# Kernel optimization log

Hardware: AMD Instinct MI355X
Metric: run time of the kernel (lower is better)

Reference implementation:

```python
import jax, jax.numpy as jnp
import numpy as np

RGB2GRAY = jnp.array([0.299, 0.587, 0.114], dtype=jnp.float32)


def _trilinear_slice(grid, z, y, x):
    """grid: (F, L, GH, GW); z,y,x: (H, W) float positions in index space
    (align_corners=True convention). Returns (H, W, F)."""
    F_, L, GH, GW = grid.shape
    z = jnp.clip(z, 0.0, L - 1)
    y = jnp.clip(y, 0.0, GH - 1)
    x = jnp.clip(x, 0.0, GW - 1)
    z0 = jnp.floor(z).astype(jnp.int32); z1 = jnp.minimum(z0 + 1, L - 1)
    y0 = jnp.floor(y).astype(jnp.int32); y1 = jnp.minimum(y0 + 1, GH - 1)
    x0 = jnp.floor(x).astype(jnp.int32); x1 = jnp.minimum(x0 + 1, GW - 1)
    wz = (z - z0)[..., None]  # (H, W, 1)
    wy = (y - y0)[..., None]
    wx = (x - x0)[..., None]

    def g(zi, yi, xi):  # gather corner -> (H, W, F)
        return jnp.moveaxis(grid[:, zi, yi, xi], 0, -1)

    c00 = g(z0, y0, x0) * (1 - wx) + g(z0, y0, x1) * wx
    c01 = g(z0, y1, x0) * (1 - wx) + g(z0, y1, x1) * wx
    c10 = g(z1, y0, x0) * (1 - wx) + g(z1, y0, x1) * wx
    c11 = g(z1, y1, x0) * (1 - wx) + g(z1, y1, x1) * wx
    c0 = c00 * (1 - wy) + c01 * wy
    c1 = c10 * (1 - wy) + c11 * wy
    return c0 * (1 - wz) + c1 * wz


def setup_inputs() -> dict:
    key = jax.random.key(0)
    k = jax.random.split(key, 5)
    H, W = 1080, 1920
    N, F_, L, GH, GW = 50, 16, 8, 16, 16
    hidden = 64
    rgb = jax.random.uniform(k[0], (H, W, 3), dtype=jnp.float32)
    grids = jax.random.normal(k[1], (N, F_, L, GH, GW), dtype=jnp.float32) * 0.1
    W1 = jax.random.normal(k[2], (hidden, F_), dtype=jnp.float32) * (1.0 / np.sqrt(F_))
    W2 = jax.random.normal(k[3], (hidden, hidden), dtype=jnp.float32) * (1.0 / np.sqrt(hidden))
    W3 = jax.random.normal(k[4], (12, hidden), dtype=jnp.float32) * (1.0 / np.sqrt(hidden))
    return {"rgb": rgb, "grids": grids, "W1": W1, "W2": W2, "W3": W3, "cam_idx": 3}


def reference(rgb, grids, W1, W2, W3, cam_idx):
    H, W, _ = rgb.shape
    _, F_, L, GH, GW = grids.shape
    grid = grids[cam_idx]  # (F, L, GH, GW)
    # guidance: gray in [0,1]; grid_sample coords in [-1,1] with align_corners=True
    # map directly to index space: pos = coord01 * (size - 1)
    gray = jnp.clip(jnp.tensordot(rgb, RGB2GRAY, axes=([-1], [0])), 0.0, 1.0)  # (H, W)
    gy = jnp.linspace(0.0, 1.0, H, dtype=jnp.float32)[:, None]  # (H, 1)
    gx = jnp.linspace(0.0, 1.0, W, dtype=jnp.float32)[None, :]  # (1, W)
    z = gray * (L - 1)
    y = jnp.broadcast_to(gy * (GH - 1), (H, W))
    x = jnp.broadcast_to(gx * (GW - 1), (H, W))
    feat = _trilinear_slice(grid, z, y, x)  # (H, W, F)
    # tiny per-pixel MLP (bias-free, torch Linear applies x @ W.T)
    h = jnp.tanh(feat @ W1.T)
    h = jnp.tanh(h @ W2.T)
    out = h @ W3.T  # (H, W, 12)
    return out.reshape(1, H, W, 3, 4)
```

## Files before the change

### kernel.cpp

```cpp
#include <hip/hip_runtime.h>

#define H_IMG 1080
#define W_IMG 1920
#define NPIX (H_IMG * W_IMG)

typedef __attribute__((ext_vector_type(8))) short bfrag8;
typedef __attribute__((ext_vector_type(4))) float facc4;

#define PK2_OFF 131072
#define PK3_OFF 147456
#define PK1_OFF 151552

__device__ __forceinline__ void split_bf16(float x, unsigned short& hi, unsigned short& lo) {
    unsigned xu = __float_as_uint(x);
    hi = (unsigned short)(xu >> 16);
    float hif = __uint_as_float(xu & 0xffff0000u);
    float lof = x - hif;
    lo = (unsigned short)(__float_as_uint(lof) >> 16);
}

__global__ void prep_kernel(const float* __restrict__ grids,
                            const int* __restrict__ cam_idx,
                            const float* __restrict__ W1,
                            const float* __restrict__ W2,
                            const float* __restrict__ W3,
                            float* __restrict__ grid_t,
                            unsigned short* __restrict__ pk1,
                            unsigned short* __restrict__ pk2,
                            unsigned short* __restrict__ pk3) {
    int idx = blockIdx.x * 256 + threadIdx.x;
    {
        int f = idx & 15, x = (idx >> 4) & 15, y = (idx >> 8) & 15, z = (idx >> 12) & 7;
        int cam = cam_idx[0];
        grid_t[idx] = grids[(((cam * 16 + f) * 8 + z) * 16 + y) * 16 + x];
    }
    if (idx < 8192) {
        int i = idx & 7, lane = (idx >> 3) & 63, h = (idx >> 9) & 1,
            s = (idx >> 10) & 1, mt = (idx >> 11) & 3;
        int j = mt * 16 + (lane & 15);
        int k = s * 32 + (lane >> 4) * 8 + i;
        unsigned short hi, lo;
        split_bf16(W2[j * 64 + k], hi, lo);
        pk2[idx] = h ? lo : hi;
    } else if (idx < 10240) {
        int e = idx - 8192;
        int i = e & 7, lane = (e >> 3) & 63, h = (e >> 9) & 1, s = (e >> 10) & 1;
        int c = lane & 15;
        int k = s * 32 + (lane >> 4) * 8 + i;
        float x = (c < 12) ? W3[c * 64 + k] : 0.0f;
        unsigned short hi, lo;
        split_bf16(x, hi, lo);
        pk3[e] = h ? lo : hi;
    } else if (idx < 14336) {
        int e = idx - 10240;
        int i = e & 7, lane = (e >> 3) & 63, h = (e >> 9) & 1, mt = (e >> 10) & 3;
        int j = mt * 16 + (lane & 15);
        int k = (lane >> 4) * 8 + i;
        float x = (k < 16) ? W1[j * 16 + k] : 0.0f;
        unsigned short hi, lo;
        split_bf16(x, hi, lo);
        pk1[e] = h ? lo : hi;
    }
}

__device__ __forceinline__ float fast_tanh(float x) {
    float e = exp2f(x * 2.8853900817779268f);
    return 1.0f - 2.0f * __builtin_amdgcn_rcpf(e + 1.0f);
}

__device__ __forceinline__ unsigned rtn_pair(float e, float o) {
    unsigned ue = __float_as_uint(e) + 0x8000u;
    unsigned uo = __float_as_uint(o) + 0x8000u;
    return __builtin_amdgcn_perm(uo, ue, 0x07060302u);
}

#define DS_FENCE() asm volatile("s_waitcnt lgkmcnt(0)" ::: "memory")
#define CBAR() asm volatile("" ::: "memory")
#define MFMA16(A, B, C) __builtin_amdgcn_mfma_f32_16x16x32_bf16((A), (B), (C), 0, 0, 0)

__global__ __launch_bounds__(256, 3)
void nbat_main(const float* __restrict__ rgb,
               const float* __restrict__ grid_t,
               const unsigned short* __restrict__ pk1,
               const unsigned short* __restrict__ pk2,
               const unsigned short* __restrict__ pk3,
               float* __restrict__ out) {
    __shared__ __align__(16) unsigned hbuf[4][3072];

    const int tid = threadIdx.x;
    const int w = tid >> 6, l = tid & 63;
    const int g = l >> 4, cc = l & 15;
    unsigned* hb = hbuf[w];
    uint4* hb4 = (uint4*)hb;
    const int H4 = 256;

    const int pixbase = blockIdx.x * 256 + w * 64;
    const int pix = pixbase + l;
    const int row = pix / W_IMG;
    const int col = pix - row * W_IMG;

    float r = rgb[3 * pix + 0];
    float gch = rgb[3 * pix + 1];
    float b = rgb[3 * pix + 2];
    float gray = fminf(fmaxf(0.299f * r + 0.587f * gch + 0.114f * b, 0.0f), 1.0f);

    float z = fminf(fmaxf(gray * 7.0f, 0.0f), 7.0f);
    float y = (float)row * (15.0f / 1079.0f);
    float x = (float)col * (15.0f / 1919.0f);

    float zf = floorf(z), yf = floorf(y), xf = floorf(x);
    int z0 = (int)zf, y0 = (int)yf, x0 = (int)xf;
    int z1 = min(z0 + 1, 7), y1 = min(y0 + 1, 15), x1 = min(x0 + 1, 15);
    float wz = z - zf, wy = y - yf, wx = x - xf;

    float feat[16];
#pragma unroll
    for (int i = 0; i < 16; ++i) feat[i] = 0.0f;

    const float4* gt4 = (const float4*)grid_t;
#pragma unroll
    for (int cz = 0; cz < 2; ++cz) {
        int zz = cz ? z1 : z0;
        float wwz = cz ? wz : (1.0f - wz);
#pragma unroll
        for (int cy = 0; cy < 2; ++cy) {
            int yy = cy ? y1 : y0;
            float wwzy = wwz * (cy ? wy : (1.0f - wy));
#pragma unroll
            for (int cx = 0; cx < 2; ++cx) {
                int xx = cx ? x1 : x0;
                float wc = wwzy * (cx ? wx : (1.0f - wx));
                int base = ((zz * 16 + yy) * 16 + xx) * 4;
#pragma unroll
                for (int q = 0; q < 4; ++q) {
                    float4 v = gt4[base + q];
                    feat[4 * q + 0] = fmaf(wc, v.x, feat[4 * q + 0]);
                    feat[4 * q + 1] = fmaf(wc, v.y, feat[4 * q + 1]);
                    feat[4 * q + 2] = fmaf(wc, v.z, feat[4 * q + 2]);
                    feat[4 * q + 3] = fmaf(wc, v.w, feat[4 * q + 3]);
                }
            }
        }
    }

    const int sl = (l >> 1) & 3;
    {
        uint4 q0, q1;
        q0.x = rtn_pair(feat[0], feat[1]);
        q0.y = rtn_pair(feat[2], feat[3]);
        q0.z = rtn_pair(feat[4], feat[5]);
        q0.w = rtn_pair(feat[6], feat[7]);
        q1.x = rtn_pair(feat[8], feat[9]);
        q1.y = rtn_pair(feat[10], feat[11]);
        q1.z = rtn_pair(feat[12], feat[13]);
        q1.w = rtn_pair(feat[14], feat[15]);
        uint4 zz4 = make_uint4(0u, 0u, 0u, 0u);
        hb4[l * 4 + (0 ^ sl)] = q0;
        hb4[l * 4 + (1 ^ sl)] = q1;
        hb4[l * 4 + (2 ^ sl)] = zz4;
        hb4[l * 4 + (3 ^ sl)] = zz4;
    }
    DS_FENCE();

    auto trans = [&](const facc4& v, int mt, int prow, int ubase)
        __attribute__((always_inline)) {
        float t0 = fast_tanh(v[0]);
        float t1 = fast_tanh(v[1]);
        float t2 = fast_tanh(v[2]);
        float t3 = fast_tanh(v[3]);
        unsigned A = rtn_pair(t0, t1);
        unsigned B = rtn_pair(t2, t3);
        int c = 2 * mt + (g >> 1);
        int u = ubase + prow * 32 + (((c ^ (prow & 7)) << 2) + ((g & 1) << 1));
        *(uint2*)(hb + u) = make_uint2(A, B);
    };

    const bfrag8* pk1v = (const bfrag8*)pk1;
    facc4 acc1[4][4];
#pragma unroll
    for (int mt = 0; mt < 4; ++mt)
#pragma unroll
        for (int nt = 0; nt < 4; ++nt) acc1[mt][nt] = (facc4){0.f, 0.f, 0.f, 0.f};
    {
        bfrag8 w1h[4], w1l[4];
#pragma unroll
        for (int mt = 0; mt < 4; ++mt) {
            w1h[mt] = pk1v[(mt * 2 + 0) * 64 + l];
            w1l[mt] = pk1v[(mt * 2 + 1) * 64 + l];
        }
#pragma unroll
        for (int nt = 0; nt < 4; ++nt) {
            int p = cc + 16 * nt;
            uint4 bq = hb4[p * 4 + (g ^ ((p >> 1) & 3))];
            bfrag8 bf = __builtin_bit_cast(bfrag8, bq);
#pragma unroll
            for (int mt = 0; mt < 4; ++mt) {
                acc1[mt][nt] = MFMA16(w1l[mt], bf, acc1[mt][nt]);
                acc1[mt][nt] = MFMA16(w1h[mt], bf, acc1[mt][nt]);
            }
        }
    }

#pragma unroll
    for (int mt = 0; mt < 4; ++mt)
#pragma unroll
        for (int nt = 0; nt < 4; ++nt) trans(acc1[mt][nt], mt, cc + 16 * nt, 1024);
    DS_FENCE();

    const bfrag8* pk2v = (const bfrag8*)pk2;
    const bfrag8* pk3v = (const bfrag8*)pk3;
#pragma unroll
    for (int h = 0; h < 2; ++h) {
        facc4 acc2[4][2];
#pragma unroll
        for (int mt = 0; mt < 4; ++mt)
#pragma unroll
            for (int ntl = 0; ntl < 2; ++ntl) acc2[mt][ntl] = (facc4){0.f, 0.f, 0.f, 0.f};
#pragma unroll
        for (int s = 0; s < 2; ++s) {
            bfrag8 w2h[4], w2l[4];
#pragma unroll
            for (int mt = 0; mt < 4; ++mt) {
                w2h[mt] = pk2v[((mt * 2 + s) * 2 + 0) * 64 + l];
                w2l[mt] = pk2v[((mt * 2 + s) * 2 + 1) * 64 + l];
            }
#pragma unroll
            for (int ntl = 0; ntl < 2; ++ntl) {
                int p = cc + 16 * (2 * h + ntl);
                uint4 q = hb4[H4 + p * 8 + ((4 * s + g) ^ (p & 7))];
                bfrag8 bh = __builtin_bit_cast(bfrag8, q);
#pragma unroll
                for (int mt = 0; mt < 4; ++mt) {
                    acc2[mt][ntl] = MFMA16(w2l[mt], bh, acc2[mt][ntl]);
                    acc2[mt][ntl] = MFMA16(w2h[mt], bh, acc2[mt][ntl]);
                }
            }
        }

#pragma unroll
        for (int mt = 0; mt < 4; ++mt)
#pragma unroll
            for (int ntl = 0; ntl < 2; ++ntl) trans(acc2[mt][ntl], mt, cc + 16 * ntl, 0);
        DS_FENCE();

        facc4 o3[2];
#pragma unroll
        for (int ntl = 0; ntl < 2; ++ntl) o3[ntl] = (facc4){0.f, 0.f, 0.f, 0.f};
#pragma unroll
        for (int s = 0; s < 2; ++s) {
            bfrag8 w3h = pk3v[(s * 2 + 0) * 64 + l];
            bfrag8 w3l = pk3v[(s * 2 + 1) * 64 + l];
#pragma unroll
            for (int ntl = 0; ntl < 2; ++ntl) {
                int pl = cc + 16 * ntl;
                uint4 q = hb4[pl * 8 + ((4 * s + g) ^ (pl & 7))];
                bfrag8 bh = __builtin_bit_cast(bfrag8, q);
                o3[ntl] = MFMA16(w3l, bh, o3[ntl]);
                o3[ntl] = MFMA16(w3h, bh, o3[ntl]);
            }
        }

        if (g < 3) {
#pragma unroll
            for (int ntl = 0; ntl < 2; ++ntl) {
                int p = pixbase + 32 * h + 16 * ntl + cc;
                *(float4*)(out + p * 12 + 4 * g) =
                    make_float4(o3[ntl][0], o3[ntl][1], o3[ntl][2], o3[ntl][3]);
            }
        }
        CBAR();
    }
}

extern "C" void kernel_launch(void* const* d_in, const int* in_sizes, int n_in,
                              void* d_out, int out_size, void* d_ws, size_t ws_size,
                              hipStream_t stream) {
    const float* rgb   = (const float*)d_in[0];
    const float* grids = (const float*)d_in[1];
    const float* W1    = (const float*)d_in[2];
    const float* W2    = (const float*)d_in[3];
    const float* W3    = (const float*)d_in[4];
    const int*   cam   = (const int*)d_in[5];

    float* grid_t = (float*)d_ws;
    unsigned short* pk2 = (unsigned short*)((char*)d_ws + PK2_OFF);
    unsigned short* pk3 = (unsigned short*)((char*)d_ws + PK3_OFF);
    unsigned short* pk1 = (unsigned short*)((char*)d_ws + PK1_OFF);

    hipLaunchKernelGGL(prep_kernel, dim3(128), dim3(256), 0, stream,
                       grids, cam, W1, W2, W3, grid_t, pk1, pk2, pk3);
    hipLaunchKernelGGL(nbat_main, dim3(NPIX / 256), dim3(256), 0, stream,
                       rgb, grid_t, pk1, pk2, pk3, (float*)d_out);
}
```

Before: 181.7 us.

## Halve pixels per wave, shrink LDS, raise occupancy, add MFMA priority hints

Each wave now handles 32 pixels instead of 64. Only half the lanes compute the trilinear features, and the two-half layer-2/3 loop is removed. The LDS buffer is halved, launch bounds go from 3 to 4 waves per SIMD, and the grid doubles. s_setprio wraps the MFMA bursts so waves in their matrix phase get issue priority. The goal is more waves in flight to hide latency, at the cost of idle lanes during the gather, twice the weight-fragment reloads per pixel, and more blocks.

```diff
diff --git a/kernel.cpp b/kernel.cpp
--- a/kernel.cpp
+++ b/kernel.cpp
@@ -75,76 +75,78 @@
 }
 
 #define DS_FENCE() asm volatile("s_waitcnt lgkmcnt(0)" ::: "memory")
-#define CBAR() asm volatile("" ::: "memory")
 #define MFMA16(A, B, C) __builtin_amdgcn_mfma_f32_16x16x32_bf16((A), (B), (C), 0, 0, 0)
-
-__global__ __launch_bounds__(256, 3)
+#define PRIO_HI() __builtin_amdgcn_s_setprio(1)
+#define PRIO_LO() __builtin_amdgcn_s_setprio(0)
+
+__global__ __launch_bounds__(256, 4)
 void nbat_main(const float* __restrict__ rgb,
                const float* __restrict__ grid_t,
                const unsigned short* __restrict__ pk1,
                const unsigned short* __restrict__ pk2,
                const unsigned short* __restrict__ pk3,
                float* __restrict__ out) {
-    __shared__ __align__(16) unsigned hbuf[4][3072];
+    __shared__ __align__(16) unsigned hbuf[4][1536];
 
     const int tid = threadIdx.x;
     const int w = tid >> 6, l = tid & 63;
     const int g = l >> 4, cc = l & 15;
     unsigned* hb = hbuf[w];
     uint4* hb4 = (uint4*)hb;
-    const int H4 = 256;
-
-    const int pixbase = blockIdx.x * 256 + w * 64;
-    const int pix = pixbase + l;
-    const int row = pix / W_IMG;
-    const int col = pix - row * W_IMG;
-
-    float r = rgb[3 * pix + 0];
-    float gch = rgb[3 * pix + 1];
-    float b = rgb[3 * pix + 2];
-    float gray = fminf(fmaxf(0.299f * r + 0.587f * gch + 0.114f * b, 0.0f), 1.0f);
-
-    float z = fminf(fmaxf(gray * 7.0f, 0.0f), 7.0f);
-    float y = (float)row * (15.0f / 1079.0f);
-    float x = (float)col * (15.0f / 1919.0f);
-
-    float zf = floorf(z), yf = floorf(y), xf = floorf(x);
-    int z0 = (int)zf, y0 = (int)yf, x0 = (int)xf;
-    int z1 = min(z0 + 1, 7), y1 = min(y0 + 1, 15), x1 = min(x0 + 1, 15);
-    float wz = z - zf, wy = y - yf, wx = x - xf;
-
-    float feat[16];
-#pragma unroll
-    for (int i = 0; i < 16; ++i) feat[i] = 0.0f;
-
-    const float4* gt4 = (const float4*)grid_t;
-#pragma unroll
-    for (int cz = 0; cz < 2; ++cz) {
-        int zz = cz ? z1 : z0;
-        float wwz = cz ? wz : (1.0f - wz);
-#pragma unroll
-        for (int cy = 0; cy < 2; ++cy) {
-            int yy = cy ? y1 : y0;
-            float wwzy = wwz * (cy ? wy : (1.0f - wy));
-#pragma unroll
-            for (int cx = 0; cx < 2; ++cx) {
-                int xx = cx ? x1 : x0;
-                float wc = wwzy * (cx ? wx : (1.0f - wx));
-                int base = ((zz * 16 + yy) * 16 + xx) * 4;
-#pragma unroll
-                for (int q = 0; q < 4; ++q) {
-                    float4 v = gt4[base + q];
-                    feat[4 * q + 0] = fmaf(wc, v.x, feat[4 * q + 0]);
-                    feat[4 * q + 1] = fmaf(wc, v.y, feat[4 * q + 1]);
-                    feat[4 * q + 2] = fmaf(wc, v.z, feat[4 * q + 2]);
-                    feat[4 * q + 3] = fmaf(wc, v.w, feat[4 * q + 3]);
+    const int HT4 = 128;
+
+    const int pixbase = blockIdx.x * 128 + w * 32;
+
+    if (l < 32) {
+        const int pix = pixbase + l;
+        const int row = pix / W_IMG;
+        const int col = pix - row * W_IMG;
+
+        float r = rgb[3 * pix + 0];
+        float gch = rgb[3 * pix + 1];
+        float b = rgb[3 * pix + 2];
+        float gray = fminf(fmaxf(0.299f * r + 0.587f * gch + 0.114f * b, 0.0f), 1.0f);
+
+        float z = fminf(fmaxf(gray * 7.0f, 0.0f), 7.0f);
+        float y = (float)row * (15.0f / 1079.0f);
+        float x = (float)col * (15.0f / 1919.0f);
+
+        float zf = floorf(z), yf = floorf(y), xf = floorf(x);
+        int z0 = (int)zf, y0 = (int)yf, x0 = (int)xf;
+        int z1 = min(z0 + 1, 7), y1 = min(y0 + 1, 15), x1 = min(x0 + 1, 15);
+        float wz = z - zf, wy = y - yf, wx = x - xf;
+
+        float feat[16];
+#pragma unroll
+        for (int i = 0; i < 16; ++i) feat[i] = 0.0f;
+
+        const float4* gt4 = (const float4*)grid_t;
+#pragma unroll
+        for (int cz = 0; cz < 2; ++cz) {
+            int zz = cz ? z1 : z0;
+            float wwz = cz ? wz : (1.0f - wz);
+#pragma unroll
+            for (int cy = 0; cy < 2; ++cy) {
+                int yy = cy ? y1 : y0;
+                float wwzy = wwz * (cy ? wy : (1.0f - wy));
+#pragma unroll
+                for (int cx = 0; cx < 2; ++cx) {
+                    int xx = cx ? x1 : x0;
+                    float wc = wwzy * (cx ? wx : (1.0f - wx));
+                    int base = ((zz * 16 + yy) * 16 + xx) * 4;
+#pragma unroll
+                    for (int q = 0; q < 4; ++q) {
+                        float4 v = gt4[base + q];
+                        feat[4 * q + 0] = fmaf(wc, v.x, feat[4 * q + 0]);
+                        feat[4 * q + 1] = fmaf(wc, v.y, feat[4 * q + 1]);
+                        feat[4 * q + 2] = fmaf(wc, v.z, feat[4 * q + 2]);
+                        feat[4 * q + 3] = fmaf(wc, v.w, feat[4 * q + 3]);
+                    }
                 }
             }
         }
-    }
-
-    const int sl = (l >> 1) & 3;
-    {
+
+        const int sl = (l >> 1) & 3;
         uint4 q0, q1;
         q0.x = rtn_pair(feat[0], feat[1]);
         q0.y = rtn_pair(feat[2], feat[3]);
@@ -162,25 +164,35 @@
     }
     DS_FENCE();
 
-    auto trans = [&](const facc4& v, int mt, int prow, int ubase)
-        __attribute__((always_inline)) {
+    bfrag8 bf[2];
+#pragma unroll
+    for (int nt = 0; nt < 2; ++nt) {
+        int p = cc + 16 * nt;
+        bf[nt] = __builtin_bit_cast(bfrag8, hb4[p * 4 + (g ^ ((p >> 1) & 3))]);
+    }
+
+    auto trans = [&](const facc4& v, int mt, int ntl) __attribute__((always_inline)) {
         float t0 = fast_tanh(v[0]);
         float t1 = fast_tanh(v[1]);
         float t2 = fast_tanh(v[2]);
         float t3 = fast_tanh(v[3]);
         unsigned A = rtn_pair(t0, t1);
         unsigned B = rtn_pair(t2, t3);
+        int p = cc + 16 * ntl;
         int c = 2 * mt + (g >> 1);
-        int u = ubase + prow * 32 + (((c ^ (prow & 7)) << 2) + ((g & 1) << 1));
+        int u = 512 + p * 32 + (((c ^ (p & 7)) << 2) + ((g & 1) << 1));
         *(uint2*)(hb + u) = make_uint2(A, B);
     };
 
     const bfrag8* pk1v = (const bfrag8*)pk1;
-    facc4 acc1[4][4];
+    const bfrag8* pk2v = (const bfrag8*)pk2;
+    const bfrag8* pk3v = (const bfrag8*)pk3;
+
+    facc4 acc1[4][2];
 #pragma unroll
     for (int mt = 0; mt < 4; ++mt)
 #pragma unroll
-        for (int nt = 0; nt < 4; ++nt) acc1[mt][nt] = (facc4){0.f, 0.f, 0.f, 0.f};
+        for (int nt = 0; nt < 2; ++nt) acc1[mt][nt] = (facc4){0.f, 0.f, 0.f, 0.f};
     {
         bfrag8 w1h[4], w1l[4];
 #pragma unroll
@@ -189,86 +201,83 @@
             w1l[mt] = pk1v[(mt * 2 + 1) * 64 + l];
         }
 #pragma unroll
-        for (int nt = 0; nt < 4; ++nt) {
-            int p = cc + 16 * nt;
-            uint4 bq = hb4[p * 4 + (g ^ ((p >> 1) & 3))];
-            bfrag8 bf = __builtin_bit_cast(bfrag8, bq);
+        for (int nt = 0; nt < 2; ++nt) {
+            PRIO_HI();
 #pragma unroll
             for (int mt = 0; mt < 4; ++mt) {
-                acc1[mt][nt] = MFMA16(w1l[mt], bf, acc1[mt][nt]);
-                acc1[mt][nt] = MFMA16(w1h[mt], bf, acc1[mt][nt]);
+                acc1[mt][nt] = MFMA16(w1l[mt], bf[nt], acc1[mt][nt]);
+                acc1[mt][nt] = MFMA16(w1h[mt], bf[nt], acc1[mt][nt]);
             }
+            PRIO_LO();
         }
     }
 
 #pragma unroll
     for (int mt = 0; mt < 4; ++mt)
 #pragma unroll
-        for (int nt = 0; nt < 4; ++nt) trans(acc1[mt][nt], mt, cc + 16 * nt, 1024);
+        for (int ntl = 0; ntl < 2; ++ntl) trans(acc1[mt][ntl], mt, ntl);
     DS_FENCE();
 
-    const bfrag8* pk2v = (const bfrag8*)pk2;
-    const bfrag8* pk3v = (const bfrag8*)pk3;
-#pragma unroll
-    for (int h = 0; h < 2; ++h) {
-        facc4 acc2[4][2];
-#pragma unroll
-        for (int mt = 0; mt < 4; ++mt)
-#pragma unroll
-            for (int ntl = 0; ntl < 2; ++ntl) acc2[mt][ntl] = (facc4){0.f, 0.f, 0.f, 0.f};
-#pragma unroll
-        for (int s = 0; s < 2; ++s) {
-            bfrag8 w2h[4], w2l[4];
+    facc4 acc2[4][2];
+#pragma unroll
+    for (int mt = 0; mt < 4; ++mt)
+#pragma unroll
+        for (int ntl = 0; ntl < 2; ++ntl) acc2[mt][ntl] = (facc4){0.f, 0.f, 0.f, 0.f};
+#pragma unroll
+    for (int s = 0; s < 2; ++s) {
+        bfrag8 w2h[4], w2l[4];
+#pragma unroll
+        for (int mt = 0; mt < 4; ++mt) {
+            w2h[mt] = pk2v[((mt * 2 + s) * 2 + 0) * 64 + l];
+            w2l[mt] = pk2v[((mt * 2 + s) * 2 + 1) * 64 + l];
+        }
+#pragma unroll
+        for (int ntl = 0; ntl < 2; ++ntl) {
+            int p = cc + 16 * ntl;
+            uint4 q = hb4[HT4 + p * 8 + ((4 * s + g) ^ (p & 7))];
+            bfrag8 bh = __builtin_bit_cast(bfrag8, q);
+            PRIO_HI();
 #pragma unroll
             for (int mt = 0; mt < 4; ++mt) {
-                w2h[mt] = pk2v[((mt * 2 + s) * 2 + 0) * 64 + l];
-                w2l[mt] = pk2v[((mt * 2 + s) * 2 + 1) * 64 + l];
+                acc2[mt][ntl] = MFMA16(w2l[mt], bh, acc2[mt][ntl]);
+                acc2[mt][ntl] = MFMA16(w2h[mt], bh, acc2[mt][ntl]);
             }
-#pragma unroll
-            for (int ntl = 0; ntl < 2; ++ntl) {
-                int p = cc + 16 * (2 * h + ntl);
-                uint4 q = hb4[H4 + p * 8 + ((4 * s + g) ^ (p & 7))];
-                bfrag8 bh = __builtin_bit_cast(bfrag8, q);
-#pragma unroll
-                for (int mt = 0; mt < 4; ++mt) {
-                    acc2[mt][ntl] = MFMA16(w2l[mt], bh, acc2[mt][ntl]);
-                    acc2[mt][ntl] = MFMA16(w2h[mt], bh, acc2[mt][ntl]);
-                }
-            }
-        }
-
-#pragma unroll
-        for (int mt = 0; mt < 4; ++mt)
-#pragma unroll
-            for (int ntl = 0; ntl < 2; ++ntl) trans(acc2[mt][ntl], mt, cc + 16 * ntl, 0);
-        DS_FENCE();
-
-        facc4 o3[2];
-#pragma unroll
-        for (int ntl = 0; ntl < 2; ++ntl) o3[ntl] = (facc4){0.f, 0.f, 0.f, 0.f};
-#pragma unroll
-        for (int s = 0; s < 2; ++s) {
-            bfrag8 w3h = pk3v[(s * 2 + 0) * 64 + l];
-            bfrag8 w3l = pk3v[(s * 2 + 1) * 64 + l];
-#pragma unroll
-            for (int ntl = 0; ntl < 2; ++ntl) {
-                int pl = cc + 16 * ntl;
-                uint4 q = hb4[pl * 8 + ((4 * s + g) ^ (pl & 7))];
-                bfrag8 bh = __builtin_bit_cast(bfrag8, q);
-                o3[ntl] = MFMA16(w3l, bh, o3[ntl]);
-                o3[ntl] = MFMA16(w3h, bh, o3[ntl]);
-            }
-        }
-
-        if (g < 3) {
-#pragma unroll
-            for (int ntl = 0; ntl < 2; ++ntl) {
-                int p = pixbase + 32 * h + 16 * ntl + cc;
-                *(float4*)(out + p * 12 + 4 * g) =
-                    make_float4(o3[ntl][0], o3[ntl][1], o3[ntl][2], o3[ntl][3]);
-            }
-        }
-        CBAR();
+            PRIO_LO();
+        }
+    }
+
+#pragma unroll
+    for (int mt = 0; mt < 4; ++mt)
+#pragma unroll
+        for (int ntl = 0; ntl < 2; ++ntl) trans(acc2[mt][ntl], mt, ntl);
+    DS_FENCE();
+
+    facc4 o3[2];
+#pragma unroll
+    for (int ntl = 0; ntl < 2; ++ntl) o3[ntl] = (facc4){0.f, 0.f, 0.f, 0.f};
+#pragma unroll
+    for (int s = 0; s < 2; ++s) {
+        bfrag8 w3h = pk3v[(s * 2 + 0) * 64 + l];
+        bfrag8 w3l = pk3v[(s * 2 + 1) * 64 + l];
+#pragma unroll
+        for (int ntl = 0; ntl < 2; ++ntl) {
+            int p = cc + 16 * ntl;
+            uint4 q = hb4[HT4 + p * 8 + ((4 * s + g) ^ (p & 7))];
+            bfrag8 bh = __builtin_bit_cast(bfrag8, q);
+            PRIO_HI();
+            o3[ntl] = MFMA16(w3l, bh, o3[ntl]);
+            o3[ntl] = MFMA16(w3h, bh, o3[ntl]);
+            PRIO_LO();
+        }
+    }
+
+    if (g < 3) {
+#pragma unroll
+        for (int ntl = 0; ntl < 2; ++ntl) {
+            int p = pixbase + 16 * ntl + cc;
+            *(float4*)(out + p * 12 + 4 * g) =
+                make_float4(o3[ntl][0], o3[ntl][1], o3[ntl][2], o3[ntl][3]);
+        }
     }
 }
 
@@ -289,6 +298,6 @@
 
     hipLaunchKernelGGL(prep_kernel, dim3(128), dim3(256), 0, stream,
                        grids, cam, W1, W2, W3, grid_t, pk1, pk2, pk3);
-    hipLaunchKernelGGL(nbat_main, dim3(NPIX / 256), dim3(256), 0, stream,
+    hipLaunchKernelGGL(nbat_main, dim3(NPIX / 128), dim3(256), 0, stream,
                        rgb, grid_t, pk1, pk2, pk3, (float*)d_out);
 }
```

Measured after the change: 181.8 us. Within noise of the previous version (+0.0%).
